# Performance work log

Measured on AMD Instinct MI355X. Metric: run time of the kernel, lower is better.

Reference implementation:

```python
import jax, jax.numpy as jnp
import numpy as np

N = 500_000          # num nodes
K = 3                # neighbors per star subgraph = graphlet_size - 1
E = N * K            # one subgraph per node -> directed (center, nbr) edges
L = 2                # hop_neighbor
FD = 2               # final_dim = 2**pqc_dim
H = 64               # hidden_dim
NC = 8               # num_classes
NIN = 16             # node_input_dim
EIN = 8              # edge_input_dim


def _lin(k, i, o):
    # torch.nn.Linear-style init scale
    return jax.random.normal(k, (i, o), jnp.float32) * (1.0 / np.sqrt(i))


def setup_inputs() -> dict:
    key = jax.random.key(0)
    ks = jax.random.split(key, 32)
    node_feat = jax.random.normal(ks[0], (N, NIN), jnp.float32)
    edge_attr = jax.random.normal(ks[1], (E, EIN), jnp.float32)
    # edge e = (center, neighbor); centers grouped: edges 3i..3i+2 belong to node i
    centers = jnp.repeat(jnp.arange(N, dtype=jnp.int32), K)
    neighbors = jax.random.randint(ks[2], (E,), 0, N, dtype=jnp.int32)
    edge_index = jnp.stack([centers, neighbors])  # [2, E]
    batch = jnp.zeros((N,), jnp.int32)
    msg_W1 = jnp.stack([_lin(ks[6 + i], 2 * FD, H) for i in range(L)])
    msg_W2 = jnp.stack([_lin(ks[8 + i], H, FD) for i in range(L)])
    upd_W1 = jnp.stack([_lin(ks[10 + i], 2 * FD, H) for i in range(L)])
    upd_W2 = jnp.stack([_lin(ks[12 + i], H, FD) for i in range(L)])
    return dict(
        node_feat=node_feat, edge_attr=edge_attr, edge_index=edge_index, batch=batch,
        Wn=_lin(ks[3], NIN, FD), bn=jnp.zeros((FD,), jnp.float32),
        We=_lin(ks[4], EIN, FD), be=jnp.zeros((FD,), jnp.float32),
        msg_W1=msg_W1, msg_b1=jnp.zeros((L, H), jnp.float32),
        msg_W2=msg_W2, msg_b2=jnp.zeros((L, FD), jnp.float32),
        upd_W1=upd_W1, upd_b1=jnp.zeros((L, H), jnp.float32),
        upd_W2=upd_W2, upd_b2=jnp.zeros((L, FD), jnp.float32),
        fin_W1=_lin(ks[14], FD, H), fin_b1=jnp.zeros((H,), jnp.float32),
        fin_W2=_lin(ks[15], H, NC), fin_b2=jnp.zeros((NC,), jnp.float32),
    )


def _leaky(x):
    return jnp.where(x >= 0, x, 0.1 * x)


def _mlp(x, W1, b1, W2, b2):
    # MLP([din, 64, dout], act=LeakyReLU(0.1)); dropout inactive at eval
    return _leaky(x @ W1 + b1) @ W2 + b2


def reference(node_feat, edge_attr, edge_index, batch, Wn, bn, We, be,
              msg_W1, msg_b1, msg_W2, msg_b2, upd_W1, upd_b1, upd_W2, upd_b2,
              fin_W1, fin_b1, fin_W2, fin_b2):
    ctr = edge_index[0]  # [E] center of each star edge
    nbr = edge_index[1]  # [E] neighbor
    h = node_feat @ Wn + bn      # [N, FD] input_node projection
    e = edge_attr @ We + be      # [E, FD] input_edge projection (fixed across layers)
    for l in range(L):
        # message over each (center, neighbor) edge: concat(edge_feat, nbr_feat)
        msg = _mlp(jnp.concatenate([e, h[nbr]], axis=1),
                   msg_W1[l], msg_b1[l], msg_W2[l], msg_b2[l])  # [E, FD]
        aggr = jax.ops.segment_sum(msg, ctr, num_segments=N)    # [N, FD]
        new = _mlp(jnp.concatenate([h, aggr], axis=1),
                   upd_W1[l], upd_b1[l], upd_W2[l], upd_b2[l])  # [N, FD]
        h = jax.nn.relu(h + new)  # updates_node[center] += new_center; then ReLU
    return _mlp(h, fin_W1, fin_b1, fin_W2, fin_b2)  # [N, NC]
```

## Files before the change

### kernel.cpp

```cpp
#include <hip/hip_runtime.h>

#define NN 500000
#define KK 3
#define EE (NN * KK)
#define HH 64
#define NC 8
#define NIN 16
#define EIN 8

typedef __attribute__((ext_vector_type(2))) _Float16 h2;
typedef __attribute__((ext_vector_type(2)))  float sf2;
typedef __attribute__((ext_vector_type(8)))  float sf8;
typedef __attribute__((ext_vector_type(16))) float sf16;

using pk_t = decltype(__builtin_amdgcn_cvt_pkrtz(0.f, 0.f));

__device__ __forceinline__ sf2 sload2(const float* p) {
    sf2 r; asm("s_load_dwordx2 %0, %1, 0x0" : "=s"(r) : "s"(p)); return r;
}
__device__ __forceinline__ sf8 sload8(const float* p) {
    sf8 r; asm("s_load_dwordx8 %0, %1, 0x0" : "=s"(r) : "s"(p)); return r;
}
__device__ __forceinline__ sf16 sload16(const float* p) {
    sf16 r; asm("s_load_dwordx16 %0, %1, 0x0" : "=s"(r) : "s"(p)); return r;
}
#define SWAIT1(a)       asm volatile("s_waitcnt lgkmcnt(0)" : "+s"(a))
#define SWAIT2(a,b)     asm volatile("s_waitcnt lgkmcnt(0)" : "+s"(a),"+s"(b))
#define SWAIT3(a,b,c)   asm volatile("s_waitcnt lgkmcnt(0)" : "+s"(a),"+s"(b),"+s"(c))
#define SWAIT5(a,b,c,d,e) asm volatile("s_waitcnt lgkmcnt(0)" : "+s"(a),"+s"(b),"+s"(c),"+s"(d),"+s"(e))

#if __has_builtin(__builtin_elementwise_fma)
#define PKFMA(a,b,c) __builtin_elementwise_fma((a),(b),(c))
#else
#define PKFMA(a,b,c) ((a)*(b)+(c))
#endif

__device__ __forceinline__ h2 bch2(float f)        { return __builtin_bit_cast(h2, f); }
__device__ __forceinline__ h2 bch2u(unsigned int u){ return __builtin_bit_cast(h2, u); }
__device__ __forceinline__ h2 dup16(float f) {
    return __builtin_bit_cast(h2, __builtin_amdgcn_cvt_pkrtz(f, f));
}
__device__ __forceinline__ float fdot2(h2 a, h2 b, float c) {
#if __has_builtin(__builtin_amdgcn_fdot2)
    return __builtin_amdgcn_fdot2(__builtin_bit_cast(pk_t, a),
                                  __builtin_bit_cast(pk_t, b), c, false);
#else
    return c + (float)a.x * (float)b.x + (float)a.y * (float)b.y;
#endif
}
__device__ __forceinline__ h2 lk2(h2 x) {
    h2 c = {(_Float16)0.1f, (_Float16)0.1f};
    return __builtin_elementwise_max(x, x * c);
}

__device__ __forceinline__ float pack2(float a, float b) {
    h2 v; v.x = (_Float16)a; v.y = (_Float16)b;
    return __builtin_bit_cast(float, v);
}

__global__ void pack_kernel(
    const float* __restrict__ msgW1, const float* __restrict__ msgb1, const float* __restrict__ msgW2,
    const float* __restrict__ updW1, const float* __restrict__ updb1, const float* __restrict__ updW2,
    const float* __restrict__ finW1, const float* __restrict__ finb1, const float* __restrict__ finW2,
    float* __restrict__ wpack)
{
    int t = threadIdx.x;
    if (t < 32) {
        int l = t >> 4, which = (t >> 3) & 1, c = t & 7;
        const float* W1 = (which ? updW1 : msgW1) + l * 4 * HH;
        const float* b1 = (which ? updb1 : msgb1) + l * HH;
        const float* W2 = (which ? updW2 : msgW2) + l * 2 * HH;
        float* dst = wpack + (l * 2 + which) * 256 + c * 32;
        int j0 = c * 8;
        for (int r = 0; r < 4; r++)
            for (int p = 0; p < 4; p++)
                dst[r * 4 + p] = pack2(W1[r * HH + j0 + 2 * p], W1[r * HH + j0 + 2 * p + 1]);
        for (int p = 0; p < 4; p++) {
            dst[16 + p] = pack2(b1[j0 + 2 * p], b1[j0 + 2 * p + 1]);
            dst[20 + p] = pack2(W2[(j0 + 2 * p) * 2 + 0], W2[(j0 + 2 * p + 1) * 2 + 0]);
            dst[24 + p] = pack2(W2[(j0 + 2 * p) * 2 + 1], W2[(j0 + 2 * p + 1) * 2 + 1]);
            dst[28 + p] = 0.0f;
        }
    } else if (t < 40) {
        int c = t - 32, j0 = c * 8;
        float* dst = wpack + 1024 + c * 48;
        for (int p = 0; p < 4; p++) {
            dst[p]      = pack2(finW1[j0 + 2 * p],      finW1[j0 + 2 * p + 1]);
            dst[4 + p]  = pack2(finW1[HH + j0 + 2 * p], finW1[HH + j0 + 2 * p + 1]);
            dst[8 + p]  = pack2(finb1[j0 + 2 * p],      finb1[j0 + 2 * p + 1]);
            dst[12 + p] = 0.0f;
        }
        for (int jp = 0; jp < 4; jp++)
            for (int cc = 0; cc < NC; cc++)
                dst[16 + jp * 8 + cc] = pack2(finW2[(j0 + 2 * jp) * NC + cc],
                                              finW2[(j0 + 2 * jp + 1) * NC + cc]);
    }
}

__global__ __launch_bounds__(256) void prep_kernel(
    const float* __restrict__ node_feat, const float* __restrict__ edge_attr,
    const float* __restrict__ Wn, const float* __restrict__ bn,
    const float* __restrict__ We, const float* __restrict__ be,
    float* __restrict__ h, unsigned int* __restrict__ ep)
{
    sf16 wn0 = sload16(Wn);
    sf16 wn1 = sload16(Wn + 16);
    sf2  bnv = sload2(bn);
    sf16 wev = sload16(We);
    sf2  bev = sload2(be);
    SWAIT5(wn0, wn1, bnv, wev, bev);

    int idx = blockIdx.x * 256 + threadIdx.x;
    if (idx < NN) {
        const float4* x4 = (const float4*)(node_feat + (size_t)idx * NIN);
        float4 v0 = x4[0], v1 = x4[1], v2 = x4[2], v3 = x4[3];
        float xs[16] = {v0.x, v0.y, v0.z, v0.w, v1.x, v1.y, v1.z, v1.w,
                        v2.x, v2.y, v2.z, v2.w, v3.x, v3.y, v3.z, v3.w};
        float a0 = bnv.x, a1 = bnv.y;
#pragma unroll
        for (int i = 0; i < 8; i++) {
            a0 = fmaf(xs[i], wn0[2 * i], a0);
            a1 = fmaf(xs[i], wn0[2 * i + 1], a1);
        }
#pragma unroll
        for (int i = 0; i < 8; i++) {
            a0 = fmaf(xs[8 + i], wn1[2 * i], a0);
            a1 = fmaf(xs[8 + i], wn1[2 * i + 1], a1);
        }
        ((float2*)h)[idx] = make_float2(a0, a1);
    } else if (idx < NN + EE) {
        int eidx = idx - NN;
        const float4* x4 = (const float4*)(edge_attr + (size_t)eidx * EIN);
        float4 v0 = x4[0], v1 = x4[1];
        float xs[8] = {v0.x, v0.y, v0.z, v0.w, v1.x, v1.y, v1.z, v1.w};
        float a0 = bev.x, a1 = bev.y;
#pragma unroll
        for (int i = 0; i < 8; i++) {
            a0 = fmaf(xs[i], wev[2 * i], a0);
            a1 = fmaf(xs[i], wev[2 * i + 1], a1);
        }
        uint2 pe;
        pe.x = __builtin_bit_cast(unsigned int, dup16(a0));
        pe.y = __builtin_bit_cast(unsigned int, dup16(a1));
        ((uint2*)ep)[eidx] = pe;
    }
}

template<bool FINAL>
__global__ __launch_bounds__(256) void layer_kernel(
    const float* __restrict__ h_in, const unsigned int* __restrict__ eP,
    const int* __restrict__ nbr,
    const float* __restrict__ mblk, const float* __restrict__ mb2,
    const float* __restrict__ ublk, const float* __restrict__ ub2,
    float* __restrict__ h_out,
    const float* __restrict__ fblk, const float* __restrict__ fb2,
    float* __restrict__ out)
{
    int i = blockIdx.x * 256 + threadIdx.x;
    if (i >= NN) return;

    sf2 mb2v = sload2(mb2);
    sf2 ub2v = sload2(ub2);
    SWAIT2(mb2v, ub2v);

    float2 hh = ((const float2*)h_in)[i];
    int base = i * KK;
    int n0 = nbr[base + 0], n1 = nbr[base + 1], n2 = nbr[base + 2];
    float2 g0 = ((const float2*)h_in)[n0];
    float2 g1 = ((const float2*)h_in)[n1];
    float2 g2 = ((const float2*)h_in)[n2];
    uint2 pe0 = ((const uint2*)eP)[base + 0];
    uint2 pe1 = ((const uint2*)eP)[base + 1];
    uint2 pe2 = ((const uint2*)eP)[base + 2];
    h2 e0x = bch2u(pe0.x), e0y = bch2u(pe0.y);
    h2 e1x = bch2u(pe1.x), e1y = bch2u(pe1.y);
    h2 e2x = bch2u(pe2.x), e2y = bch2u(pe2.y);
    h2 n0x = dup16(g0.x), n0y = dup16(g0.y);
    h2 n1x = dup16(g1.x), n1y = dup16(g1.y);
    h2 n2x = dup16(g2.x), n2y = dup16(g2.y);

    float a0 = 3.0f * mb2v.x, a1 = 3.0f * mb2v.y;
#pragma unroll 1
    for (int c = 0; c < 8; c++) {
        sf16 A = sload16(mblk + c * 32);
        sf16 B = sload16(mblk + c * 32 + 16);
        SWAIT2(A, B);
#pragma unroll
        for (int jp = 0; jp < 4; jp++) {
            h2 w0 = bch2(A[jp]), w1 = bch2(A[4 + jp]);
            h2 w2 = bch2(A[8 + jp]), w3 = bch2(A[12 + jp]);
            h2 bb = bch2(B[jp]);
            h2 t0 = PKFMA(e0x, w0, PKFMA(e0y, w1, PKFMA(n0x, w2, PKFMA(n0y, w3, bb))));
            h2 t1 = PKFMA(e1x, w0, PKFMA(e1y, w1, PKFMA(n1x, w2, PKFMA(n1y, w3, bb))));
            h2 t2 = PKFMA(e2x, w0, PKFMA(e2y, w1, PKFMA(n2x, w2, PKFMA(n2y, w3, bb))));
            h2 ts = lk2(t0) + lk2(t1) + lk2(t2);
            a0 = fdot2(ts, bch2(B[4 + jp]), a0);
            a1 = fdot2(ts, bch2(B[8 + jp]), a1);
        }
    }

    h2 hx = dup16(hh.x), hy = dup16(hh.y), ax = dup16(a0), ay = dup16(a1);
    float u0 = ub2v.x, u1 = ub2v.y;
#pragma unroll 1
    for (int c = 0; c < 8; c++) {
        sf16 A = sload16(ublk + c * 32);
        sf16 B = sload16(ublk + c * 32 + 16);
        SWAIT2(A, B);
#pragma unroll
        for (int jp = 0; jp < 4; jp++) {
            h2 tt = PKFMA(hx, bch2(A[jp]),
                    PKFMA(hy, bch2(A[4 + jp]),
                    PKFMA(ax, bch2(A[8 + jp]),
                    PKFMA(ay, bch2(A[12 + jp]), bch2(B[jp])))));
            tt = lk2(tt);
            u0 = fdot2(tt, bch2(B[4 + jp]), u0);
            u1 = fdot2(tt, bch2(B[8 + jp]), u1);
        }
    }
    float nh0 = fmaxf(hh.x + u0, 0.0f);
    float nh1 = fmaxf(hh.y + u1, 0.0f);

    if (!FINAL) {
        ((float2*)h_out)[i] = make_float2(nh0, nh1);
    } else {
        sf8 fb2v = sload8(fb2);
        SWAIT1(fb2v);
        float o[NC];
#pragma unroll
        for (int cc = 0; cc < NC; cc++) o[cc] = fb2v[cc];
        h2 nx = dup16(nh0), ny = dup16(nh1);
#pragma unroll 1
        for (int c = 0; c < 8; c++) {
            sf16 A = sload16(fblk + c * 48);
            sf16 B = sload16(fblk + c * 48 + 16);
            sf16 C = sload16(fblk + c * 48 + 32);
            SWAIT3(A, B, C);
#pragma unroll
            for (int jp = 0; jp < 4; jp++) {
                h2 tt = lk2(PKFMA(nx, bch2(A[jp]), PKFMA(ny, bch2(A[4 + jp]), bch2(A[8 + jp]))));
#pragma unroll
                for (int cc = 0; cc < NC; cc++) {
                    float w = (jp < 2) ? B[(jp & 1) * 8 + cc] : C[(jp & 1) * 8 + cc];
                    o[cc] = fdot2(tt, bch2(w), o[cc]);
                }
            }
        }
        float4* op = (float4*)(out + (size_t)i * NC);
        op[0] = make_float4(o[0], o[1], o[2], o[3]);
        op[1] = make_float4(o[4], o[5], o[6], o[7]);
    }
}

extern "C" void kernel_launch(void* const* d_in, const int* in_sizes, int n_in,
                              void* d_out, int out_size, void* d_ws, size_t ws_size,
                              hipStream_t stream) {
    const float* node_feat = (const float*)d_in[0];
    const float* edge_attr = (const float*)d_in[1];
    const int* edge_index = (const int*)d_in[2];
    const float* Wn = (const float*)d_in[4];
    const float* bn = (const float*)d_in[5];
    const float* We = (const float*)d_in[6];
    const float* be = (const float*)d_in[7];
    const float* msgW1 = (const float*)d_in[8];
    const float* msgb1 = (const float*)d_in[9];
    const float* msgW2 = (const float*)d_in[10];
    const float* msgb2 = (const float*)d_in[11];
    const float* updW1 = (const float*)d_in[12];
    const float* updb1 = (const float*)d_in[13];
    const float* updW2 = (const float*)d_in[14];
    const float* updb2 = (const float*)d_in[15];
    const float* finW1 = (const float*)d_in[16];
    const float* finb1 = (const float*)d_in[17];
    const float* finW2 = (const float*)d_in[18];
    const float* finb2 = (const float*)d_in[19];
    float* out = (float*)d_out;

    const int* nbr = edge_index + EE;

    char* ws = (char*)d_ws;
    float* hA = (float*)ws;
    float* hB = (float*)(ws + (size_t)NN * 2 * 4);
    unsigned int* eP = (unsigned int*)(ws + (size_t)NN * 4 * 4);
    float* wpack = (float*)(ws + (size_t)NN * 4 * 4 + (size_t)EE * 2 * 4);

    pack_kernel<<<1, 64, 0, stream>>>(msgW1, msgb1, msgW2,
                                      updW1, updb1, updW2,
                                      finW1, finb1, finW2, wpack);

    const int threads = 256;
    int prep_grid = (NN + EE + threads - 1) / threads;
    prep_kernel<<<prep_grid, threads, 0, stream>>>(node_feat, edge_attr, Wn, bn, We, be, hA, eP);

    int grid = (NN + threads - 1) / threads;
    layer_kernel<false><<<grid, threads, 0, stream>>>(
        hA, eP, nbr,
        wpack + 0 * 256, msgb2,
        wpack + 1 * 256, updb2,
        hB, wpack + 1024, finb2, nullptr);
    layer_kernel<true><<<grid, threads, 0, stream>>>(
        hB, eP, nbr,
        wpack + 2 * 256, msgb2 + 2,
        wpack + 3 * 256, updb2 + 2,
        nullptr, wpack + 1024, finb2, out);
}
```

Before: 204.7 us.

## Store node and edge features as packed fp16 and process two nodes per thread

Node hidden states and edge projections are now kept as one packed fp16x2 word instead of fp32 pairs or duplicated halves, which halves the gather and stream traffic. Each layer thread now handles two nodes half the array apart, so each scalar-loaded weight chunk is reused across both nodes. Weight loads are also batched two chunks per wait. The weight-pack kernel is folded into block 0 of the prep kernel, saving a launch. Storing h in fp16 between layers adds rounding error, and doubling the per-thread work raises register pressure.

```diff
diff --git a/kernel.cpp b/kernel.cpp
--- a/kernel.cpp
+++ b/kernel.cpp
@@ -1,6 +1,7 @@
 #include <hip/hip_runtime.h>
 
 #define NN 500000
+#define HALF 250000
 #define KK 3
 #define EE (NN * KK)
 #define HH 64
@@ -24,9 +25,10 @@
 __device__ __forceinline__ sf16 sload16(const float* p) {
     sf16 r; asm("s_load_dwordx16 %0, %1, 0x0" : "=s"(r) : "s"(p)); return r;
 }
-#define SWAIT1(a)       asm volatile("s_waitcnt lgkmcnt(0)" : "+s"(a))
-#define SWAIT2(a,b)     asm volatile("s_waitcnt lgkmcnt(0)" : "+s"(a),"+s"(b))
-#define SWAIT3(a,b,c)   asm volatile("s_waitcnt lgkmcnt(0)" : "+s"(a),"+s"(b),"+s"(c))
+#define SWAIT1(a)         asm volatile("s_waitcnt lgkmcnt(0)" : "+s"(a))
+#define SWAIT2(a,b)       asm volatile("s_waitcnt lgkmcnt(0)" : "+s"(a),"+s"(b))
+#define SWAIT3(a,b,c)     asm volatile("s_waitcnt lgkmcnt(0)" : "+s"(a),"+s"(b),"+s"(c))
+#define SWAIT4(a,b,c,d)   asm volatile("s_waitcnt lgkmcnt(0)" : "+s"(a),"+s"(b),"+s"(c),"+s"(d))
 #define SWAIT5(a,b,c,d,e) asm volatile("s_waitcnt lgkmcnt(0)" : "+s"(a),"+s"(b),"+s"(c),"+s"(d),"+s"(e))
 
 #if __has_builtin(__builtin_elementwise_fma)
@@ -40,6 +42,18 @@
 __device__ __forceinline__ h2 dup16(float f) {
     return __builtin_bit_cast(h2, __builtin_amdgcn_cvt_pkrtz(f, f));
 }
+__device__ __forceinline__ unsigned int pkrtz_u(float a, float b) {
+    return __builtin_bit_cast(unsigned int, __builtin_amdgcn_cvt_pkrtz(a, b));
+}
+__device__ __forceinline__ h2 splat_lo(unsigned int u) {
+    h2 p = bch2u(u); h2 r; r.x = p.x; r.y = p.x; return r;
+}
+__device__ __forceinline__ h2 splat_hi(unsigned int u) {
+    h2 p = bch2u(u); h2 r; r.x = p.y; r.y = p.y; return r;
+}
+__device__ __forceinline__ float lo_f32(unsigned int u) { return (float)bch2u(u).x; }
+__device__ __forceinline__ float hi_f32(unsigned int u) { return (float)bch2u(u).y; }
+
 __device__ __forceinline__ float fdot2(h2 a, h2 b, float c) {
 #if __has_builtin(__builtin_amdgcn_fdot2)
     return __builtin_amdgcn_fdot2(__builtin_bit_cast(pk_t, a),
@@ -52,56 +66,20 @@
     h2 c = {(_Float16)0.1f, (_Float16)0.1f};
     return __builtin_elementwise_max(x, x * c);
 }
-
 __device__ __forceinline__ float pack2(float a, float b) {
     h2 v; v.x = (_Float16)a; v.y = (_Float16)b;
     return __builtin_bit_cast(float, v);
 }
 
-__global__ void pack_kernel(
+__global__ __launch_bounds__(256) void prep_kernel(
+    const float* __restrict__ node_feat, const float* __restrict__ edge_attr,
+    const float* __restrict__ Wn, const float* __restrict__ bn,
+    const float* __restrict__ We, const float* __restrict__ be,
+    unsigned int* __restrict__ hp, unsigned int* __restrict__ ep,
     const float* __restrict__ msgW1, const float* __restrict__ msgb1, const float* __restrict__ msgW2,
     const float* __restrict__ updW1, const float* __restrict__ updb1, const float* __restrict__ updW2,
     const float* __restrict__ finW1, const float* __restrict__ finb1, const float* __restrict__ finW2,
     float* __restrict__ wpack)
-{
-    int t = threadIdx.x;
-    if (t < 32) {
-        int l = t >> 4, which = (t >> 3) & 1, c = t & 7;
-        const float* W1 = (which ? updW1 : msgW1) + l * 4 * HH;
-        const float* b1 = (which ? updb1 : msgb1) + l * HH;
-        const float* W2 = (which ? updW2 : msgW2) + l * 2 * HH;
-        float* dst = wpack + (l * 2 + which) * 256 + c * 32;
-        int j0 = c * 8;
-        for (int r = 0; r < 4; r++)
-            for (int p = 0; p < 4; p++)
-                dst[r * 4 + p] = pack2(W1[r * HH + j0 + 2 * p], W1[r * HH + j0 + 2 * p + 1]);
-        for (int p = 0; p < 4; p++) {
-            dst[16 + p] = pack2(b1[j0 + 2 * p], b1[j0 + 2 * p + 1]);
-            dst[20 + p] = pack2(W2[(j0 + 2 * p) * 2 + 0], W2[(j0 + 2 * p + 1) * 2 + 0]);
-            dst[24 + p] = pack2(W2[(j0 + 2 * p) * 2 + 1], W2[(j0 + 2 * p + 1) * 2 + 1]);
-            dst[28 + p] = 0.0f;
-        }
-    } else if (t < 40) {
-        int c = t - 32, j0 = c * 8;
-        float* dst = wpack + 1024 + c * 48;
-        for (int p = 0; p < 4; p++) {
-            dst[p]      = pack2(finW1[j0 + 2 * p],      finW1[j0 + 2 * p + 1]);
-            dst[4 + p]  = pack2(finW1[HH + j0 + 2 * p], finW1[HH + j0 + 2 * p + 1]);
-            dst[8 + p]  = pack2(finb1[j0 + 2 * p],      finb1[j0 + 2 * p + 1]);
-            dst[12 + p] = 0.0f;
-        }
-        for (int jp = 0; jp < 4; jp++)
-            for (int cc = 0; cc < NC; cc++)
-                dst[16 + jp * 8 + cc] = pack2(finW2[(j0 + 2 * jp) * NC + cc],
-                                              finW2[(j0 + 2 * jp + 1) * NC + cc]);
-    }
-}
-
-__global__ __launch_bounds__(256) void prep_kernel(
-    const float* __restrict__ node_feat, const float* __restrict__ edge_attr,
-    const float* __restrict__ Wn, const float* __restrict__ bn,
-    const float* __restrict__ We, const float* __restrict__ be,
-    float* __restrict__ h, unsigned int* __restrict__ ep)
 {
     sf16 wn0 = sload16(Wn);
     sf16 wn1 = sload16(Wn + 16);
@@ -127,7 +105,7 @@
             a0 = fmaf(xs[8 + i], wn1[2 * i], a0);
             a1 = fmaf(xs[8 + i], wn1[2 * i + 1], a1);
         }
-        ((float2*)h)[idx] = make_float2(a0, a1);
+        hp[idx] = pkrtz_u(a0, a1);
     } else if (idx < NN + EE) {
         int eidx = idx - NN;
         const float4* x4 = (const float4*)(edge_attr + (size_t)eidx * EIN);
@@ -139,96 +117,168 @@
             a0 = fmaf(xs[i], wev[2 * i], a0);
             a1 = fmaf(xs[i], wev[2 * i + 1], a1);
         }
-        uint2 pe;
-        pe.x = __builtin_bit_cast(unsigned int, dup16(a0));
-        pe.y = __builtin_bit_cast(unsigned int, dup16(a1));
-        ((uint2*)ep)[eidx] = pe;
+        ep[eidx] = pkrtz_u(a0, a1);
+    }
+
+    if (blockIdx.x == 0) {
+        int t = threadIdx.x;
+        if (t < 32) {
+            int l = t >> 4, which = (t >> 3) & 1, c = t & 7;
+            const float* W1 = (which ? updW1 : msgW1) + l * 4 * HH;
+            const float* b1 = (which ? updb1 : msgb1) + l * HH;
+            const float* W2 = (which ? updW2 : msgW2) + l * 2 * HH;
+            float* dst = wpack + (l * 2 + which) * 256 + c * 32;
+            int j0 = c * 8;
+            for (int r = 0; r < 4; r++)
+                for (int p = 0; p < 4; p++)
+                    dst[r * 4 + p] = pack2(W1[r * HH + j0 + 2 * p], W1[r * HH + j0 + 2 * p + 1]);
+            for (int p = 0; p < 4; p++) {
+                dst[16 + p] = pack2(b1[j0 + 2 * p], b1[j0 + 2 * p + 1]);
+                dst[20 + p] = pack2(W2[(j0 + 2 * p) * 2 + 0], W2[(j0 + 2 * p + 1) * 2 + 0]);
+                dst[24 + p] = pack2(W2[(j0 + 2 * p) * 2 + 1], W2[(j0 + 2 * p + 1) * 2 + 1]);
+                dst[28 + p] = 0.0f;
+            }
+        } else if (t < 40) {
+            int c = t - 32, j0 = c * 8;
+            float* dst = wpack + 1024 + c * 48;
+            for (int p = 0; p < 4; p++) {
+                dst[p]      = pack2(finW1[j0 + 2 * p],      finW1[j0 + 2 * p + 1]);
+                dst[4 + p]  = pack2(finW1[HH + j0 + 2 * p], finW1[HH + j0 + 2 * p + 1]);
+                dst[8 + p]  = pack2(finb1[j0 + 2 * p],      finb1[j0 + 2 * p + 1]);
+                dst[12 + p] = 0.0f;
+            }
+            for (int jp = 0; jp < 4; jp++)
+                for (int cc = 0; cc < NC; cc++)
+                    dst[16 + jp * 8 + cc] = pack2(finW2[(j0 + 2 * jp) * NC + cc],
+                                                  finW2[(j0 + 2 * jp + 1) * NC + cc]);
+        }
     }
 }
 
 template<bool FINAL>
 __global__ __launch_bounds__(256) void layer_kernel(
-    const float* __restrict__ h_in, const unsigned int* __restrict__ eP,
+    const unsigned int* __restrict__ hp_in, const unsigned int* __restrict__ eP,
     const int* __restrict__ nbr,
     const float* __restrict__ mblk, const float* __restrict__ mb2,
     const float* __restrict__ ublk, const float* __restrict__ ub2,
-    float* __restrict__ h_out,
+    unsigned int* __restrict__ hp_out,
     const float* __restrict__ fblk, const float* __restrict__ fb2,
     float* __restrict__ out)
 {
-    int i = blockIdx.x * 256 + threadIdx.x;
-    if (i >= NN) return;
+    int tA = blockIdx.x * 256 + threadIdx.x;
+    if (tA >= HALF) return;
+    int iA = tA, iB = tA + HALF;
 
     sf2 mb2v = sload2(mb2);
     sf2 ub2v = sload2(ub2);
     SWAIT2(mb2v, ub2v);
 
-    float2 hh = ((const float2*)h_in)[i];
-    int base = i * KK;
-    int n0 = nbr[base + 0], n1 = nbr[base + 1], n2 = nbr[base + 2];
-    float2 g0 = ((const float2*)h_in)[n0];
-    float2 g1 = ((const float2*)h_in)[n1];
-    float2 g2 = ((const float2*)h_in)[n2];
-    uint2 pe0 = ((const uint2*)eP)[base + 0];
-    uint2 pe1 = ((const uint2*)eP)[base + 1];
-    uint2 pe2 = ((const uint2*)eP)[base + 2];
-    h2 e0x = bch2u(pe0.x), e0y = bch2u(pe0.y);
-    h2 e1x = bch2u(pe1.x), e1y = bch2u(pe1.y);
-    h2 e2x = bch2u(pe2.x), e2y = bch2u(pe2.y);
-    h2 n0x = dup16(g0.x), n0y = dup16(g0.y);
-    h2 n1x = dup16(g1.x), n1y = dup16(g1.y);
-    h2 n2x = dup16(g2.x), n2y = dup16(g2.y);
-
-    float a0 = 3.0f * mb2v.x, a1 = 3.0f * mb2v.y;
+    unsigned int hA = hp_in[iA], hB = hp_in[iB];
+    int baseA = iA * KK, baseB = iB * KK;
+    int nA0 = nbr[baseA], nA1 = nbr[baseA + 1], nA2 = nbr[baseA + 2];
+    int nB0 = nbr[baseB], nB1 = nbr[baseB + 1], nB2 = nbr[baseB + 2];
+    unsigned int gA0 = hp_in[nA0], gA1 = hp_in[nA1], gA2 = hp_in[nA2];
+    unsigned int gB0 = hp_in[nB0], gB1 = hp_in[nB1], gB2 = hp_in[nB2];
+    unsigned int eA0 = eP[baseA], eA1 = eP[baseA + 1], eA2 = eP[baseA + 2];
+    unsigned int eB0 = eP[baseB], eB1 = eP[baseB + 1], eB2 = eP[baseB + 2];
+
+    h2 eA0x = splat_lo(eA0), eA0y = splat_hi(eA0);
+    h2 eA1x = splat_lo(eA1), eA1y = splat_hi(eA1);
+    h2 eA2x = splat_lo(eA2), eA2y = splat_hi(eA2);
+    h2 eB0x = splat_lo(eB0), eB0y = splat_hi(eB0);
+    h2 eB1x = splat_lo(eB1), eB1y = splat_hi(eB1);
+    h2 eB2x = splat_lo(eB2), eB2y = splat_hi(eB2);
+    h2 nA0x = splat_lo(gA0), nA0y = splat_hi(gA0);
+    h2 nA1x = splat_lo(gA1), nA1y = splat_hi(gA1);
+    h2 nA2x = splat_lo(gA2), nA2y = splat_hi(gA2);
+    h2 nB0x = splat_lo(gB0), nB0y = splat_hi(gB0);
+    h2 nB1x = splat_lo(gB1), nB1y = splat_hi(gB1);
+    h2 nB2x = splat_lo(gB2), nB2y = splat_hi(gB2);
+
+    float a0A = 3.0f * mb2v.x, a1A = 3.0f * mb2v.y;
+    float a0B = a0A, a1B = a1A;
 #pragma unroll 1
-    for (int c = 0; c < 8; c++) {
-        sf16 A = sload16(mblk + c * 32);
-        sf16 B = sload16(mblk + c * 32 + 16);
-        SWAIT2(A, B);
-#pragma unroll
-        for (int jp = 0; jp < 4; jp++) {
-            h2 w0 = bch2(A[jp]), w1 = bch2(A[4 + jp]);
-            h2 w2 = bch2(A[8 + jp]), w3 = bch2(A[12 + jp]);
-            h2 bb = bch2(B[jp]);
-            h2 t0 = PKFMA(e0x, w0, PKFMA(e0y, w1, PKFMA(n0x, w2, PKFMA(n0y, w3, bb))));
-            h2 t1 = PKFMA(e1x, w0, PKFMA(e1y, w1, PKFMA(n1x, w2, PKFMA(n1y, w3, bb))));
-            h2 t2 = PKFMA(e2x, w0, PKFMA(e2y, w1, PKFMA(n2x, w2, PKFMA(n2y, w3, bb))));
-            h2 ts = lk2(t0) + lk2(t1) + lk2(t2);
-            a0 = fdot2(ts, bch2(B[4 + jp]), a0);
-            a1 = fdot2(ts, bch2(B[8 + jp]), a1);
-        }
-    }
-
-    h2 hx = dup16(hh.x), hy = dup16(hh.y), ax = dup16(a0), ay = dup16(a1);
-    float u0 = ub2v.x, u1 = ub2v.y;
+    for (int c = 0; c < 8; c += 2) {
+        sf16 A0 = sload16(mblk + c * 32);
+        sf16 B0 = sload16(mblk + c * 32 + 16);
+        sf16 A1 = sload16(mblk + c * 32 + 32);
+        sf16 B1 = sload16(mblk + c * 32 + 48);
+        SWAIT4(A0, B0, A1, B1);
+#pragma unroll
+        for (int half = 0; half < 2; half++) {
+            const sf16& A = half ? A1 : A0;
+            const sf16& B = half ? B1 : B0;
+#pragma unroll
+            for (int jp = 0; jp < 4; jp++) {
+                h2 w0 = bch2(A[jp]), w1 = bch2(A[4 + jp]);
+                h2 w2 = bch2(A[8 + jp]), w3 = bch2(A[12 + jp]);
+                h2 bb = bch2(B[jp]);
+                h2 wcx = bch2(B[4 + jp]), wcy = bch2(B[8 + jp]);
+                h2 t0 = PKFMA(eA0x, w0, PKFMA(eA0y, w1, PKFMA(nA0x, w2, PKFMA(nA0y, w3, bb))));
+                h2 t1 = PKFMA(eA1x, w0, PKFMA(eA1y, w1, PKFMA(nA1x, w2, PKFMA(nA1y, w3, bb))));
+                h2 t2 = PKFMA(eA2x, w0, PKFMA(eA2y, w1, PKFMA(nA2x, w2, PKFMA(nA2y, w3, bb))));
+                h2 tsA = lk2(t0) + lk2(t1) + lk2(t2);
+                a0A = fdot2(tsA, wcx, a0A);
+                a1A = fdot2(tsA, wcy, a1A);
+                h2 s0 = PKFMA(eB0x, w0, PKFMA(eB0y, w1, PKFMA(nB0x, w2, PKFMA(nB0y, w3, bb))));
+                h2 s1 = PKFMA(eB1x, w0, PKFMA(eB1y, w1, PKFMA(nB1x, w2, PKFMA(nB1y, w3, bb))));
+                h2 s2 = PKFMA(eB2x, w0, PKFMA(eB2y, w1, PKFMA(nB2x, w2, PKFMA(nB2y, w3, bb))));
+                h2 tsB = lk2(s0) + lk2(s1) + lk2(s2);
+                a0B = fdot2(tsB, wcx, a0B);
+                a1B = fdot2(tsB, wcy, a1B);
+            }
+        }
+    }
+
+    h2 hAx = splat_lo(hA), hAy = splat_hi(hA);
+    h2 hBx = splat_lo(hB), hBy = splat_hi(hB);
+    h2 aAx = dup16(a0A), aAy = dup16(a1A);
+    h2 aBx = dup16(a0B), aBy = dup16(a1B);
+    float u0A = ub2v.x, u1A = ub2v.y, u0B = ub2v.x, u1B = ub2v.y;
 #pragma unroll 1
-    for (int c = 0; c < 8; c++) {
-        sf16 A = sload16(ublk + c * 32);
-        sf16 B = sload16(ublk + c * 32 + 16);
-        SWAIT2(A, B);
-#pragma unroll
-        for (int jp = 0; jp < 4; jp++) {
-            h2 tt = PKFMA(hx, bch2(A[jp]),
-                    PKFMA(hy, bch2(A[4 + jp]),
-                    PKFMA(ax, bch2(A[8 + jp]),
-                    PKFMA(ay, bch2(A[12 + jp]), bch2(B[jp])))));
-            tt = lk2(tt);
-            u0 = fdot2(tt, bch2(B[4 + jp]), u0);
-            u1 = fdot2(tt, bch2(B[8 + jp]), u1);
-        }
-    }
-    float nh0 = fmaxf(hh.x + u0, 0.0f);
-    float nh1 = fmaxf(hh.y + u1, 0.0f);
-
-    if (!FINAL) {
-        ((float2*)h_out)[i] = make_float2(nh0, nh1);
+    for (int c = 0; c < 8; c += 2) {
+        sf16 A0 = sload16(ublk + c * 32);
+        sf16 B0 = sload16(ublk + c * 32 + 16);
+        sf16 A1 = sload16(ublk + c * 32 + 32);
+        sf16 B1 = sload16(ublk + c * 32 + 48);
+        SWAIT4(A0, B0, A1, B1);
+#pragma unroll
+        for (int half = 0; half < 2; half++) {
+            const sf16& A = half ? A1 : A0;
+            const sf16& B = half ? B1 : B0;
+#pragma unroll
+            for (int jp = 0; jp < 4; jp++) {
+                h2 w0 = bch2(A[jp]), w1 = bch2(A[4 + jp]);
+                h2 w2 = bch2(A[8 + jp]), w3 = bch2(A[12 + jp]);
+                h2 bb = bch2(B[jp]);
+                h2 wcx = bch2(B[4 + jp]), wcy = bch2(B[8 + jp]);
+                h2 tt = PKFMA(hAx, w0, PKFMA(hAy, w1, PKFMA(aAx, w2, PKFMA(aAy, w3, bb))));
+                tt = lk2(tt);
+                u0A = fdot2(tt, wcx, u0A);
+                u1A = fdot2(tt, wcy, u1A);
+                h2 ss = PKFMA(hBx, w0, PKFMA(hBy, w1, PKFMA(aBx, w2, PKFMA(aBy, w3, bb))));
+                ss = lk2(ss);
+                u0B = fdot2(ss, wcx, u0B);
+                u1B = fdot2(ss, wcy, u1B);
+            }
+        }
+    }
+    float nhA0 = fmaxf(lo_f32(hA) + u0A, 0.0f);
+    float nhA1 = fmaxf(hi_f32(hA) + u1A, 0.0f);
+    float nhB0 = fmaxf(lo_f32(hB) + u0B, 0.0f);
+    float nhB1 = fmaxf(hi_f32(hB) + u1B, 0.0f);
+
+    if constexpr (!FINAL) {
+        hp_out[iA] = pkrtz_u(nhA0, nhA1);
+        hp_out[iB] = pkrtz_u(nhB0, nhB1);
     } else {
         sf8 fb2v = sload8(fb2);
         SWAIT1(fb2v);
-        float o[NC];
-#pragma unroll
-        for (int cc = 0; cc < NC; cc++) o[cc] = fb2v[cc];
-        h2 nx = dup16(nh0), ny = dup16(nh1);
+        float oA[NC], oB[NC];
+#pragma unroll
+        for (int cc = 0; cc < NC; cc++) { oA[cc] = fb2v[cc]; oB[cc] = fb2v[cc]; }
+        h2 nAx = dup16(nhA0), nAy = dup16(nhA1);
+        h2 nBx = dup16(nhB0), nBy = dup16(nhB1);
 #pragma unroll 1
         for (int c = 0; c < 8; c++) {
             sf16 A = sload16(fblk + c * 48);
@@ -237,17 +287,24 @@
             SWAIT3(A, B, C);
 #pragma unroll
             for (int jp = 0; jp < 4; jp++) {
-                h2 tt = lk2(PKFMA(nx, bch2(A[jp]), PKFMA(ny, bch2(A[4 + jp]), bch2(A[8 + jp]))));
+                h2 w1a = bch2(A[jp]), w1b = bch2(A[4 + jp]), bb = bch2(A[8 + jp]);
+                h2 ttA = lk2(PKFMA(nAx, w1a, PKFMA(nAy, w1b, bb)));
+                h2 ttB = lk2(PKFMA(nBx, w1a, PKFMA(nBy, w1b, bb)));
 #pragma unroll
                 for (int cc = 0; cc < NC; cc++) {
                     float w = (jp < 2) ? B[(jp & 1) * 8 + cc] : C[(jp & 1) * 8 + cc];
-                    o[cc] = fdot2(tt, bch2(w), o[cc]);
+                    h2 wv = bch2(w);
+                    oA[cc] = fdot2(ttA, wv, oA[cc]);
+                    oB[cc] = fdot2(ttB, wv, oB[cc]);
                 }
             }
         }
-        float4* op = (float4*)(out + (size_t)i * NC);
-        op[0] = make_float4(o[0], o[1], o[2], o[3]);
-        op[1] = make_float4(o[4], o[5], o[6], o[7]);
+        float4* opA = (float4*)(out + (size_t)iA * NC);
+        opA[0] = make_float4(oA[0], oA[1], oA[2], oA[3]);
+        opA[1] = make_float4(oA[4], oA[5], oA[6], oA[7]);
+        float4* opB = (float4*)(out + (size_t)iB * NC);
+        opB[0] = make_float4(oB[0], oB[1], oB[2], oB[3]);
+        opB[1] = make_float4(oB[4], oB[5], oB[6], oB[7]);
     }
 }
 
@@ -278,20 +335,19 @@
     const int* nbr = edge_index + EE;
 
     char* ws = (char*)d_ws;
-    float* hA = (float*)ws;
-    float* hB = (float*)(ws + (size_t)NN * 2 * 4);
-    unsigned int* eP = (unsigned int*)(ws + (size_t)NN * 4 * 4);
-    float* wpack = (float*)(ws + (size_t)NN * 4 * 4 + (size_t)EE * 2 * 4);
-
-    pack_kernel<<<1, 64, 0, stream>>>(msgW1, msgb1, msgW2,
-                                      updW1, updb1, updW2,
-                                      finW1, finb1, finW2, wpack);
+    unsigned int* hA = (unsigned int*)ws;
+    unsigned int* hB = (unsigned int*)(ws + (size_t)NN * 4);
+    unsigned int* eP = (unsigned int*)(ws + (size_t)NN * 8);
+    float* wpack = (float*)(ws + (size_t)NN * 8 + (size_t)EE * 4);
 
     const int threads = 256;
     int prep_grid = (NN + EE + threads - 1) / threads;
-    prep_kernel<<<prep_grid, threads, 0, stream>>>(node_feat, edge_attr, Wn, bn, We, be, hA, eP);
-
-    int grid = (NN + threads - 1) / threads;
+    prep_kernel<<<prep_grid, threads, 0, stream>>>(
+        node_feat, edge_attr, Wn, bn, We, be, hA, eP,
+        msgW1, msgb1, msgW2, updW1, updb1, updW2,
+        finW1, finb1, finW2, wpack);
+
+    int grid = (HALF + threads - 1) / threads;
     layer_kernel<false><<<grid, threads, 0, stream>>>(
         hA, eP, nbr,
         wpack + 0 * 256, msgb2,
```

Result: faster. 198.4 us (-3.0%).

## Store node and edge features as packed fp16 and fold weight packing into prep

Applied to the files above, without the earlier changes.

Node hidden state and edge projections are now stored as a single packed half2 word per element instead of float2 or duplicated half pairs, halving gather and stream traffic in the layer kernels. The weight-packing kernel is merged into block 0 of the prep kernel, removing one launch. The MLP chunk loops issue two chunks of scalar weight loads per wait. Keeping the hidden state in fp16 between layers adds rounding error to the residual path.

```diff
diff --git a/kernel.cpp b/kernel.cpp
--- a/kernel.cpp
+++ b/kernel.cpp
@@ -24,9 +24,10 @@
 __device__ __forceinline__ sf16 sload16(const float* p) {
     sf16 r; asm("s_load_dwordx16 %0, %1, 0x0" : "=s"(r) : "s"(p)); return r;
 }
-#define SWAIT1(a)       asm volatile("s_waitcnt lgkmcnt(0)" : "+s"(a))
-#define SWAIT2(a,b)     asm volatile("s_waitcnt lgkmcnt(0)" : "+s"(a),"+s"(b))
-#define SWAIT3(a,b,c)   asm volatile("s_waitcnt lgkmcnt(0)" : "+s"(a),"+s"(b),"+s"(c))
+#define SWAIT1(a)         asm volatile("s_waitcnt lgkmcnt(0)" : "+s"(a))
+#define SWAIT2(a,b)       asm volatile("s_waitcnt lgkmcnt(0)" : "+s"(a),"+s"(b))
+#define SWAIT3(a,b,c)     asm volatile("s_waitcnt lgkmcnt(0)" : "+s"(a),"+s"(b),"+s"(c))
+#define SWAIT4(a,b,c,d)   asm volatile("s_waitcnt lgkmcnt(0)" : "+s"(a),"+s"(b),"+s"(c),"+s"(d))
 #define SWAIT5(a,b,c,d,e) asm volatile("s_waitcnt lgkmcnt(0)" : "+s"(a),"+s"(b),"+s"(c),"+s"(d),"+s"(e))
 
 #if __has_builtin(__builtin_elementwise_fma)
@@ -40,6 +41,18 @@
 __device__ __forceinline__ h2 dup16(float f) {
     return __builtin_bit_cast(h2, __builtin_amdgcn_cvt_pkrtz(f, f));
 }
+__device__ __forceinline__ unsigned int pkrtz_u(float a, float b) {
+    return __builtin_bit_cast(unsigned int, __builtin_amdgcn_cvt_pkrtz(a, b));
+}
+__device__ __forceinline__ h2 splat_lo(unsigned int u) {
+    h2 p = bch2u(u); h2 r; r.x = p.x; r.y = p.x; return r;
+}
+__device__ __forceinline__ h2 splat_hi(unsigned int u) {
+    h2 p = bch2u(u); h2 r; r.x = p.y; r.y = p.y; return r;
+}
+__device__ __forceinline__ float lo_f32(unsigned int u) { return (float)bch2u(u).x; }
+__device__ __forceinline__ float hi_f32(unsigned int u) { return (float)bch2u(u).y; }
+
 __device__ __forceinline__ float fdot2(h2 a, h2 b, float c) {
 #if __has_builtin(__builtin_amdgcn_fdot2)
     return __builtin_amdgcn_fdot2(__builtin_bit_cast(pk_t, a),
@@ -52,56 +65,20 @@
     h2 c = {(_Float16)0.1f, (_Float16)0.1f};
     return __builtin_elementwise_max(x, x * c);
 }
-
 __device__ __forceinline__ float pack2(float a, float b) {
     h2 v; v.x = (_Float16)a; v.y = (_Float16)b;
     return __builtin_bit_cast(float, v);
 }
 
-__global__ void pack_kernel(
+__global__ __launch_bounds__(256) void prep_kernel(
+    const float* __restrict__ node_feat, const float* __restrict__ edge_attr,
+    const float* __restrict__ Wn, const float* __restrict__ bn,
+    const float* __restrict__ We, const float* __restrict__ be,
+    unsigned int* __restrict__ hp, unsigned int* __restrict__ ep,
     const float* __restrict__ msgW1, const float* __restrict__ msgb1, const float* __restrict__ msgW2,
     const float* __restrict__ updW1, const float* __restrict__ updb1, const float* __restrict__ updW2,
     const float* __restrict__ finW1, const float* __restrict__ finb1, const float* __restrict__ finW2,
     float* __restrict__ wpack)
-{
-    int t = threadIdx.x;
-    if (t < 32) {
-        int l = t >> 4, which = (t >> 3) & 1, c = t & 7;
-        const float* W1 = (which ? updW1 : msgW1) + l * 4 * HH;
-        const float* b1 = (which ? updb1 : msgb1) + l * HH;
-        const float* W2 = (which ? updW2 : msgW2) + l * 2 * HH;
-        float* dst = wpack + (l * 2 + which) * 256 + c * 32;
-        int j0 = c * 8;
-        for (int r = 0; r < 4; r++)
-            for (int p = 0; p < 4; p++)
-                dst[r * 4 + p] = pack2(W1[r * HH + j0 + 2 * p], W1[r * HH + j0 + 2 * p + 1]);
-        for (int p = 0; p < 4; p++) {
-            dst[16 + p] = pack2(b1[j0 + 2 * p], b1[j0 + 2 * p + 1]);
-            dst[20 + p] = pack2(W2[(j0 + 2 * p) * 2 + 0], W2[(j0 + 2 * p + 1) * 2 + 0]);
-            dst[24 + p] = pack2(W2[(j0 + 2 * p) * 2 + 1], W2[(j0 + 2 * p + 1) * 2 + 1]);
-            dst[28 + p] = 0.0f;
-        }
-    } else if (t < 40) {
-        int c = t - 32, j0 = c * 8;
-        float* dst = wpack + 1024 + c * 48;
-        for (int p = 0; p < 4; p++) {
-            dst[p]      = pack2(finW1[j0 + 2 * p],      finW1[j0 + 2 * p + 1]);
-            dst[4 + p]  = pack2(finW1[HH + j0 + 2 * p], finW1[HH + j0 + 2 * p + 1]);
-            dst[8 + p]  = pack2(finb1[j0 + 2 * p],      finb1[j0 + 2 * p + 1]);
-            dst[12 + p] = 0.0f;
-        }
-        for (int jp = 0; jp < 4; jp++)
-            for (int cc = 0; cc < NC; cc++)
-                dst[16 + jp * 8 + cc] = pack2(finW2[(j0 + 2 * jp) * NC + cc],
-                                              finW2[(j0 + 2 * jp + 1) * NC + cc]);
-    }
-}
-
-__global__ __launch_bounds__(256) void prep_kernel(
-    const float* __restrict__ node_feat, const float* __restrict__ edge_attr,
-    const float* __restrict__ Wn, const float* __restrict__ bn,
-    const float* __restrict__ We, const float* __restrict__ be,
-    float* __restrict__ h, unsigned int* __restrict__ ep)
 {
     sf16 wn0 = sload16(Wn);
     sf16 wn1 = sload16(Wn + 16);
@@ -127,7 +104,7 @@
             a0 = fmaf(xs[8 + i], wn1[2 * i], a0);
             a1 = fmaf(xs[8 + i], wn1[2 * i + 1], a1);
         }
-        ((float2*)h)[idx] = make_float2(a0, a1);
+        hp[idx] = pkrtz_u(a0, a1);
     } else if (idx < NN + EE) {
         int eidx = idx - NN;
         const float4* x4 = (const float4*)(edge_attr + (size_t)eidx * EIN);
@@ -139,20 +116,51 @@
             a0 = fmaf(xs[i], wev[2 * i], a0);
             a1 = fmaf(xs[i], wev[2 * i + 1], a1);
         }
-        uint2 pe;
-        pe.x = __builtin_bit_cast(unsigned int, dup16(a0));
-        pe.y = __builtin_bit_cast(unsigned int, dup16(a1));
-        ((uint2*)ep)[eidx] = pe;
+        ep[eidx] = pkrtz_u(a0, a1);
+    }
+
+    if (blockIdx.x == 0) {
+        int t = threadIdx.x;
+        if (t < 32) {
+            int l = t >> 4, which = (t >> 3) & 1, c = t & 7;
+            const float* W1 = (which ? updW1 : msgW1) + l * 4 * HH;
+            const float* b1 = (which ? updb1 : msgb1) + l * HH;
+            const float* W2 = (which ? updW2 : msgW2) + l * 2 * HH;
+            float* dst = wpack + (l * 2 + which) * 256 + c * 32;
+            int j0 = c * 8;
+            for (int r = 0; r < 4; r++)
+                for (int p = 0; p < 4; p++)
+                    dst[r * 4 + p] = pack2(W1[r * HH + j0 + 2 * p], W1[r * HH + j0 + 2 * p + 1]);
+            for (int p = 0; p < 4; p++) {
+                dst[16 + p] = pack2(b1[j0 + 2 * p], b1[j0 + 2 * p + 1]);
+                dst[20 + p] = pack2(W2[(j0 + 2 * p) * 2 + 0], W2[(j0 + 2 * p + 1) * 2 + 0]);
+                dst[24 + p] = pack2(W2[(j0 + 2 * p) * 2 + 1], W2[(j0 + 2 * p + 1) * 2 + 1]);
+                dst[28 + p] = 0.0f;
+            }
+        } else if (t < 40) {
+            int c = t - 32, j0 = c * 8;
+            float* dst = wpack + 1024 + c * 48;
+            for (int p = 0; p < 4; p++) {
+                dst[p]      = pack2(finW1[j0 + 2 * p],      finW1[j0 + 2 * p + 1]);
+                dst[4 + p]  = pack2(finW1[HH + j0 + 2 * p], finW1[HH + j0 + 2 * p + 1]);
+                dst[8 + p]  = pack2(finb1[j0 + 2 * p],      finb1[j0 + 2 * p + 1]);
+                dst[12 + p] = 0.0f;
+            }
+            for (int jp = 0; jp < 4; jp++)
+                for (int cc = 0; cc < NC; cc++)
+                    dst[16 + jp * 8 + cc] = pack2(finW2[(j0 + 2 * jp) * NC + cc],
+                                                  finW2[(j0 + 2 * jp + 1) * NC + cc]);
+        }
     }
 }
 
 template<bool FINAL>
 __global__ __launch_bounds__(256) void layer_kernel(
-    const float* __restrict__ h_in, const unsigned int* __restrict__ eP,
+    const unsigned int* __restrict__ hp_in, const unsigned int* __restrict__ eP,
     const int* __restrict__ nbr,
     const float* __restrict__ mblk, const float* __restrict__ mb2,
     const float* __restrict__ ublk, const float* __restrict__ ub2,
-    float* __restrict__ h_out,
+    unsigned int* __restrict__ hp_out,
     const float* __restrict__ fblk, const float* __restrict__ fb2,
     float* __restrict__ out)
 {
@@ -163,65 +171,77 @@
     sf2 ub2v = sload2(ub2);
     SWAIT2(mb2v, ub2v);
 
-    float2 hh = ((const float2*)h_in)[i];
+    unsigned int hO = hp_in[i];
     int base = i * KK;
     int n0 = nbr[base + 0], n1 = nbr[base + 1], n2 = nbr[base + 2];
-    float2 g0 = ((const float2*)h_in)[n0];
-    float2 g1 = ((const float2*)h_in)[n1];
-    float2 g2 = ((const float2*)h_in)[n2];
-    uint2 pe0 = ((const uint2*)eP)[base + 0];
-    uint2 pe1 = ((const uint2*)eP)[base + 1];
-    uint2 pe2 = ((const uint2*)eP)[base + 2];
-    h2 e0x = bch2u(pe0.x), e0y = bch2u(pe0.y);
-    h2 e1x = bch2u(pe1.x), e1y = bch2u(pe1.y);
-    h2 e2x = bch2u(pe2.x), e2y = bch2u(pe2.y);
-    h2 n0x = dup16(g0.x), n0y = dup16(g0.y);
-    h2 n1x = dup16(g1.x), n1y = dup16(g1.y);
-    h2 n2x = dup16(g2.x), n2y = dup16(g2.y);
+    unsigned int g0 = hp_in[n0], g1 = hp_in[n1], g2 = hp_in[n2];
+    unsigned int e0 = eP[base + 0], e1 = eP[base + 1], e2 = eP[base + 2];
+
+    h2 e0x = splat_lo(e0), e0y = splat_hi(e0);
+    h2 e1x = splat_lo(e1), e1y = splat_hi(e1);
+    h2 e2x = splat_lo(e2), e2y = splat_hi(e2);
+    h2 n0x = splat_lo(g0), n0y = splat_hi(g0);
+    h2 n1x = splat_lo(g1), n1y = splat_hi(g1);
+    h2 n2x = splat_lo(g2), n2y = splat_hi(g2);
 
     float a0 = 3.0f * mb2v.x, a1 = 3.0f * mb2v.y;
 #pragma unroll 1
-    for (int c = 0; c < 8; c++) {
-        sf16 A = sload16(mblk + c * 32);
-        sf16 B = sload16(mblk + c * 32 + 16);
-        SWAIT2(A, B);
-#pragma unroll
-        for (int jp = 0; jp < 4; jp++) {
-            h2 w0 = bch2(A[jp]), w1 = bch2(A[4 + jp]);
-            h2 w2 = bch2(A[8 + jp]), w3 = bch2(A[12 + jp]);
-            h2 bb = bch2(B[jp]);
-            h2 t0 = PKFMA(e0x, w0, PKFMA(e0y, w1, PKFMA(n0x, w2, PKFMA(n0y, w3, bb))));
-            h2 t1 = PKFMA(e1x, w0, PKFMA(e1y, w1, PKFMA(n1x, w2, PKFMA(n1y, w3, bb))));
-            h2 t2 = PKFMA(e2x, w0, PKFMA(e2y, w1, PKFMA(n2x, w2, PKFMA(n2y, w3, bb))));
-            h2 ts = lk2(t0) + lk2(t1) + lk2(t2);
-            a0 = fdot2(ts, bch2(B[4 + jp]), a0);
-            a1 = fdot2(ts, bch2(B[8 + jp]), a1);
-        }
-    }
-
-    h2 hx = dup16(hh.x), hy = dup16(hh.y), ax = dup16(a0), ay = dup16(a1);
+    for (int c = 0; c < 8; c += 2) {
+        sf16 A0 = sload16(mblk + c * 32);
+        sf16 B0 = sload16(mblk + c * 32 + 16);
+        sf16 A1 = sload16(mblk + c * 32 + 32);
+        sf16 B1 = sload16(mblk + c * 32 + 48);
+        SWAIT4(A0, B0, A1, B1);
+#pragma unroll
+        for (int half = 0; half < 2; half++) {
+            const sf16& A = half ? A1 : A0;
+            const sf16& B = half ? B1 : B0;
+#pragma unroll
+            for (int jp = 0; jp < 4; jp++) {
+                h2 w0 = bch2(A[jp]), w1 = bch2(A[4 + jp]);
+                h2 w2 = bch2(A[8 + jp]), w3 = bch2(A[12 + jp]);
+                h2 bb = bch2(B[jp]);
+                h2 t0 = PKFMA(e0x, w0, PKFMA(e0y, w1, PKFMA(n0x, w2, PKFMA(n0y, w3, bb))));
+                h2 t1 = PKFMA(e1x, w0, PKFMA(e1y, w1, PKFMA(n1x, w2, PKFMA(n1y, w3, bb))));
+                h2 t2 = PKFMA(e2x, w0, PKFMA(e2y, w1, PKFMA(n2x, w2, PKFMA(n2y, w3, bb))));
+                h2 ts = lk2(t0) + lk2(t1) + lk2(t2);
+                a0 = fdot2(ts, bch2(B[4 + jp]), a0);
+                a1 = fdot2(ts, bch2(B[8 + jp]), a1);
+            }
+        }
+    }
+
+    h2 hx = splat_lo(hO), hy = splat_hi(hO);
+    h2 ax = dup16(a0), ay = dup16(a1);
     float u0 = ub2v.x, u1 = ub2v.y;
 #pragma unroll 1
-    for (int c = 0; c < 8; c++) {
-        sf16 A = sload16(ublk + c * 32);
-        sf16 B = sload16(ublk + c * 32 + 16);
-        SWAIT2(A, B);
-#pragma unroll
-        for (int jp = 0; jp < 4; jp++) {
-            h2 tt = PKFMA(hx, bch2(A[jp]),
-                    PKFMA(hy, bch2(A[4 + jp]),
-                    PKFMA(ax, bch2(A[8 + jp]),
-                    PKFMA(ay, bch2(A[12 + jp]), bch2(B[jp])))));
-            tt = lk2(tt);
-            u0 = fdot2(tt, bch2(B[4 + jp]), u0);
-            u1 = fdot2(tt, bch2(B[8 + jp]), u1);
-        }
-    }
-    float nh0 = fmaxf(hh.x + u0, 0.0f);
-    float nh1 = fmaxf(hh.y + u1, 0.0f);
-
-    if (!FINAL) {
-        ((float2*)h_out)[i] = make_float2(nh0, nh1);
+    for (int c = 0; c < 8; c += 2) {
+        sf16 A0 = sload16(ublk + c * 32);
+        sf16 B0 = sload16(ublk + c * 32 + 16);
+        sf16 A1 = sload16(ublk + c * 32 + 32);
+        sf16 B1 = sload16(ublk + c * 32 + 48);
+        SWAIT4(A0, B0, A1, B1);
+#pragma unroll
+        for (int half = 0; half < 2; half++) {
+            const sf16& A = half ? A1 : A0;
+            const sf16& B = half ? B1 : B0;
+#pragma unroll
+            for (int jp = 0; jp < 4; jp++) {
+                h2 tt = PKFMA(hx, bch2(A[jp]),
+                        PKFMA(hy, bch2(A[4 + jp]),
+                        PKFMA(ax, bch2(A[8 + jp]),
+                        PKFMA(ay, bch2(A[12 + jp]), bch2(B[jp])))));
+                tt = lk2(tt);
+                u0 = fdot2(tt, bch2(B[4 + jp]), u0);
+                u1 = fdot2(tt, bch2(B[8 + jp]), u1);
+            }
+        }
+    }
+    float nh0 = fmaxf(lo_f32(hO) + u0, 0.0f);
+    float nh1 = fmaxf(hi_f32(hO) + u1, 0.0f);
+
+    if constexpr (!FINAL) {
+        hp_out[i] = pkrtz_u(nh0, nh1);
     } else {
         sf8 fb2v = sload8(fb2);
         SWAIT1(fb2v);
@@ -237,7 +257,8 @@
             SWAIT3(A, B, C);
 #pragma unroll
             for (int jp = 0; jp < 4; jp++) {
-                h2 tt = lk2(PKFMA(nx, bch2(A[jp]), PKFMA(ny, bch2(A[4 + jp]), bch2(A[8 + jp]))));
+                h2 w1a = bch2(A[jp]), w1b = bch2(A[4 + jp]), bb = bch2(A[8 + jp]);
+                h2 tt = lk2(PKFMA(nx, w1a, PKFMA(ny, w1b, bb)));
 #pragma unroll
                 for (int cc = 0; cc < NC; cc++) {
                     float w = (jp < 2) ? B[(jp & 1) * 8 + cc] : C[(jp & 1) * 8 + cc];
@@ -278,18 +299,17 @@
     const int* nbr = edge_index + EE;
 
     char* ws = (char*)d_ws;
-    float* hA = (float*)ws;
-    float* hB = (float*)(ws + (size_t)NN * 2 * 4);
-    unsigned int* eP = (unsigned int*)(ws + (size_t)NN * 4 * 4);
-    float* wpack = (float*)(ws + (size_t)NN * 4 * 4 + (size_t)EE * 2 * 4);
-
-    pack_kernel<<<1, 64, 0, stream>>>(msgW1, msgb1, msgW2,
-                                      updW1, updb1, updW2,
-                                      finW1, finb1, finW2, wpack);
+    unsigned int* hA = (unsigned int*)ws;
+    unsigned int* hB = (unsigned int*)(ws + (size_t)NN * 4);
+    unsigned int* eP = (unsigned int*)(ws + (size_t)NN * 8);
+    float* wpack = (float*)(ws + (size_t)NN * 8 + (size_t)EE * 4);
 
     const int threads = 256;
     int prep_grid = (NN + EE + threads - 1) / threads;
-    prep_kernel<<<prep_grid, threads, 0, stream>>>(node_feat, edge_attr, Wn, bn, We, be, hA, eP);
+    prep_kernel<<<prep_grid, threads, 0, stream>>>(
+        node_feat, edge_attr, Wn, bn, We, be, hA, eP,
+        msgW1, msgb1, msgW2, updW1, updb1, updW2,
+        finW1, finb1, finW2, wpack);
 
     int grid = (NN + threads - 1) / threads;
     layer_kernel<false><<<grid, threads, 0, stream>>>(
```

After: 197.4 us. -3.6%, faster.
